# Kernel tuning notes

Hardware: AMD Instinct MI355X
Metric: run time of the kernel (lower is better)

The kernel has to match this reference:

```python
import jax, jax.numpy as jnp
import numpy as np

N_NODES = 10000
N_EDGES = 100000
MUL = 32        # multiplicity of 0e and 1o in node feats / out irreps
ATTR = 16       # node_attrs scalars
RADIAL = 8      # edge_feats scalars
W_NUMEL = 4 * MUL * MUL  # 4 CG paths, fully-connected [mul1=32, mul2=1, mul_out=32]


def setup_inputs() -> dict:
    key = jax.random.key(0)
    ks = jax.random.split(key, 12)
    return {
        'node_attrs': jax.random.normal(ks[0], (N_NODES, ATTR), jnp.float32),
        'node_feats': jax.random.normal(ks[1], (N_NODES, 4 * MUL), jnp.float32),  # 32x0e | 32x1o flattened
        'edge_attrs': jax.random.normal(ks[2], (N_EDGES, 4), jnp.float32),        # Y0 | Y1 (3 comps)
        'edge_feats': jax.random.normal(ks[3], (N_EDGES, RADIAL), jnp.float32),
        'edge_index': jax.random.randint(ks[4], (2, N_EDGES), 0, N_NODES, jnp.int32),
        'Wgen': jax.random.normal(ks[5], (RADIAL, W_NUMEL), jnp.float32),  # conv_tp_weights (o3.Linear on scalars)
        'L1s': jax.random.normal(ks[6], (MUL, MUL), jnp.float32),  # linear_1, scalar block
        'L1v': jax.random.normal(ks[7], (MUL, MUL), jnp.float32),  # linear_1, vector block
        'WS0': jax.random.normal(ks[8], (MUL, ATTR, MUL), jnp.float32),  # skip_tp 0e*0e->0e
        'WS1': jax.random.normal(ks[9], (MUL, ATTR, MUL), jnp.float32),  # skip_tp 1o*0e->1o
        'L2s': jax.random.normal(ks[10], (MUL, MUL), jnp.float32),
        'L2v': jax.random.normal(ks[11], (MUL, MUL), jnp.float32),
    }


def reference(node_attrs, node_feats, edge_attrs, edge_feats, edge_index,
              Wgen, L1s, L1v, WS0, WS1, L2s, L2v):
    sender, receiver = edge_index[0], edge_index[1]
    n = node_attrs.shape[0]

    # gather sender node feats, split irreps: [E,32] scalars, [E,32,3] vectors
    g = node_feats[sender]
    xs = g[:, :MUL]
    xv = g[:, MUL:].reshape(-1, MUL, 3)
    ys = edge_attrs[:, 0]    # l=0 edge attr
    yv = edge_attrs[:, 1:]   # l=1 edge attr, [E,3]

    # per-edge generated tensor-product weights (o3.Linear on scalar edge feats)
    tw = (edge_feats @ Wgen) * (1.0 / np.sqrt(RADIAL))
    tw = tw.reshape(-1, 4, MUL, MUL)
    WA, WB, WC, WD = tw[:, 0], tw[:, 1], tw[:, 2], tw[:, 3]

    # fully-connected CG tensor product (4 paths, edge attrs have mul=1)
    outA = jnp.einsum('euw,eu,e->ew', WA, xs, ys)          # 0e x 0e -> 0e
    outB = jnp.einsum('euw,eu,ei->ewi', WB, xs, yv)        # 0e x 1o -> 1o
    outC = jnp.einsum('euw,eui,e->ewi', WC, xv, ys)        # 1o x 0e -> 1o
    dot = jnp.einsum('eui,ei->eu', xv, yv) * (1.0 / np.sqrt(3.0))  # CG for 1o x 1o -> 0e
    outD = jnp.einsum('euw,eu->ew', WD, dot)
    alpha = 1.0 / np.sqrt(2 * MUL)  # fan-in path normalization (2 paths x mul1=32 per output irrep)
    ms = (outA + outD) * alpha      # [E,32]
    mv = (outB + outC) * alpha      # [E,32,3]

    # linear_1 (per-irrep mixing)
    lnorm = 1.0 / np.sqrt(MUL)
    ms = (ms @ L1s) * lnorm
    mv = jnp.einsum('ewi,wu->eui', mv, L1v) * lnorm

    # scatter-sum messages to receiver nodes
    Ms = jax.ops.segment_sum(ms, receiver, num_segments=n)   # [N,32]
    Mv = jax.ops.segment_sum(mv, receiver, num_segments=n)   # [N,32,3]

    # skip_tp: out irreps x node_attrs (16x0e) -> out irreps
    snorm = 1.0 / np.sqrt(MUL * ATTR)
    ss = jnp.einsum('uvw,nu,nv->nw', WS0, Ms, node_attrs) * snorm
    sv = jnp.einsum('uvw,nui,nv->nwi', WS1, Mv, node_attrs) * snorm

    # linear_2
    ss = (ss @ L2s) * lnorm
    sv = jnp.einsum('nwi,wu->nui', sv, L2v) * lnorm

    # residual, flatten irreps back to [N, 128]
    return jnp.concatenate([Ms + ss, (Mv + sv).reshape(n, 3 * MUL)], axis=1)
```

## Files before the change

### kernel.cpp

```cpp
#include <hip/hip_runtime.h>
#include <hip/hip_bf16.h>

#define N_NODES 10000
#define N_EDGES 100000
#define SLOTS 40

typedef __attribute__((ext_vector_type(8))) short short8;
typedef __attribute__((ext_vector_type(4))) short shortx4;
typedef __attribute__((ext_vector_type(4))) float f32x4;

static __device__ inline short bf16bits(float x) {
    union { __bf16 b; short s; } u;
    u.b = (__bf16)x;
    return u.s;
}
static __device__ inline unsigned short bf16u(float x) {
    union { __bf16 b; unsigned short s; } u;
    u.b = (__bf16)x;
    return u.s;
}
static __device__ inline float bf2f(unsigned short us) {
    union { unsigned int u; float f; } c;
    c.u = ((unsigned int)us) << 16;
    return c.f;
}
static __device__ inline short8 cvt8(const float* f) {
    short8 r;
#pragma unroll
    for (int j = 0; j < 8; ++j) r[j] = bf16bits(f[j]);
    return r;
}

__global__ __launch_bounds__(1024) void prep_kernel(
    const float* __restrict__ Wgen, const float* __restrict__ L1s,
    const float* __restrict__ L1v, const float* __restrict__ WS0,
    const float* __restrict__ WS1, const float* __restrict__ L2s,
    const float* __restrict__ L2v, unsigned short* __restrict__ Wc,
    unsigned short* __restrict__ WB0, unsigned short* __restrict__ WB1,
    int* __restrict__ cnt) {
    const float S = 1.0f / 128.0f;
    int tid = blockIdx.x * 1024 + threadIdx.x;
    if (tid < N_NODES) cnt[tid] = 0;
    if (tid < 32768) {
        int j = tid & 7;
        int lane = (tid >> 3) & 63;
        int ks = (tid >> 9) & 7;
        int nt = tid >> 12;
        int col = nt * 16 + (lane & 15);
        int u = (lane >> 4) * 8 + j;
        int r = ks;
        int p, c2;
        const float* M;
        float sc = S;
        if (col < 32)      { p = 0; M = L1s; c2 = col; }
        else if (col < 64) { p = 1; M = L1v; c2 = col - 32; }
        else if (col < 96) { p = 2; M = L1v; c2 = col - 64; }
        else               { p = 3; M = L1s; c2 = col - 96; sc = S * 0.57735026918962576f; }
        const float* wg = Wgen + r * 4096 + p * 1024 + u * 32;
        float acc = 0.f;
#pragma unroll
        for (int w = 0; w < 32; ++w) acc += wg[w] * M[w * 32 + c2];
        Wc[tid] = bf16u(acc * sc);
    } else {
        int idx = tid - 32768;
        int table = idx >> 14;
        int r14 = idx & 16383;
        int j = r14 & 7;
        int lane = (r14 >> 3) & 63;
        int ks = (r14 >> 9) & 15;
        int k = ks * 32 + (lane >> 4) * 8 + j;
        int u = k >> 4, v = k & 15;
        int w = ((r14 >> 13) & 1) * 16 + (lane & 15);
        const float* WS = table ? WS1 : WS0;
        const float* L2 = table ? L2v : L2s;
        const float* src = WS + u * 512 + v * 32;
        float acc = 0.f;
#pragma unroll
        for (int x = 0; x < 32; ++x) acc += src[x] * L2[x * 32 + w];
        unsigned short val = bf16u(acc * S);
        if (table) WB1[r14] = val; else WB0[r14] = val;
    }
}

__global__ __launch_bounds__(256) void edge_kernel(
    const float* __restrict__ node_feats, const float* __restrict__ edge_attrs,
    const float* __restrict__ edge_feats, const int* __restrict__ edge_index,
    const unsigned short* __restrict__ Wc, int* __restrict__ cnt,
    unsigned short* __restrict__ Msg) {
    __shared__ short8 sW8[4096];
    __shared__ int sSL[4][16];
    __shared__ f32x4 sEA[4][16];
    {
        const short8* src = (const short8*)Wc;
        for (int i = threadIdx.x; i < 4096; i += 256) sW8[i] = src[i];
    }
    __syncthreads();

    const int lane = threadIdx.x & 63;
    const int m = lane & 15, q = lane >> 4;
    const int wv = threadIdx.x >> 6;
    const int wave = (blockIdx.x * 256 + threadIdx.x) >> 6;
    const int stride = gridDim.x * 4;
    const int NT = N_EDGES / 16;

    int tile = wave;
    if (tile >= NT) return;

    float xsC[8], xvC[24], efC[8];
    f32x4 eaC;
    int slC = 0;

    {
        int e = tile * 16 + m;
        int snd = edge_index[e];
        if (lane < 16) {
            int r = edge_index[N_EDGES + e];
            slC = r * SLOTS + atomicAdd(&cnt[r], 1);
        }
        const float* g = node_feats + snd * 128;
        *(f32x4*)&xsC[0] = *(const f32x4*)(g + q * 8);
        *(f32x4*)&xsC[4] = *(const f32x4*)(g + q * 8 + 4);
#pragma unroll
        for (int i = 0; i < 6; ++i)
            *(f32x4*)&xvC[i * 4] = *(const f32x4*)(g + 32 + q * 24 + i * 4);
        *(f32x4*)&efC[0] = *(const f32x4*)(edge_feats + e * 8);
        *(f32x4*)&efC[4] = *(const f32x4*)(edge_feats + e * 8 + 4);
        eaC = *(const f32x4*)(edge_attrs + e * 4);
    }
    int snd1 = 0, rcv1 = 0;
    {
        int t1 = tile + stride;
        if (t1 < NT) {
            int e1 = t1 * 16 + m;
            snd1 = edge_index[e1];
            if (lane < 16) rcv1 = edge_index[N_EDGES + e1];
        }
    }

    while (tile < NT) {
        const int tn = tile + stride;
        const bool hasN = tn < NT;
        const int t2 = tile + 2 * stride;
        const bool has2 = t2 < NT;

        if (lane < 16) {
            sSL[wv][lane] = slC;
            sEA[wv][lane] = eaC;
        }

        float xsN[8], xvN[24], efN[8];
        f32x4 eaN;
        int slN = 0;
        if (hasN) {
            int en = tn * 16 + m;
            if (lane < 16) slN = rcv1 * SLOTS + atomicAdd(&cnt[rcv1], 1);
            const float* gN = node_feats + snd1 * 128;
            *(f32x4*)&xsN[0] = *(const f32x4*)(gN + q * 8);
            *(f32x4*)&xsN[4] = *(const f32x4*)(gN + q * 8 + 4);
#pragma unroll
            for (int i = 0; i < 6; ++i)
                *(f32x4*)&xvN[i * 4] = *(const f32x4*)(gN + 32 + q * 24 + i * 4);
            *(f32x4*)&efN[0] = *(const f32x4*)(edge_feats + en * 8);
            *(f32x4*)&efN[4] = *(const f32x4*)(edge_feats + en * 8 + 4);
            eaN = *(const f32x4*)(edge_attrs + en * 4);
        }

        int snd2 = 0, rcv2 = 0;
        if (has2) {
            int e2 = t2 * 16 + m;
            snd2 = edge_index[e2];
            if (lane < 16) rcv2 = edge_index[N_EDGES + e2];
        }

        float dt[8];
        {
            float y0 = eaC.y, y1 = eaC.z, y2 = eaC.w;
#pragma unroll
            for (int j = 0; j < 8; ++j)
                dt[j] = xvC[j * 3] * y0 + xvC[j * 3 + 1] * y1 + xvC[j * 3 + 2] * y2;
        }

        f32x4 z = {0.f, 0.f, 0.f, 0.f};
        f32x4 fA[2] = {z, z}, fB[2] = {z, z}, fD[2] = {z, z};
        f32x4 fC[3][2] = {{z, z}, {z, z}, {z, z}};

#pragma unroll
        for (int ks = 0; ks < 8; ++ks) {
            float h = efC[ks];
            float t[8];
#pragma unroll
            for (int j = 0; j < 8; ++j) t[j] = h * xsC[j];
            {
                short8 a = cvt8(t);
                fA[0] = __builtin_amdgcn_mfma_f32_16x16x32_bf16(a, sW8[(0 * 8 + ks) * 64 + lane], fA[0], 0, 0, 0);
                fA[1] = __builtin_amdgcn_mfma_f32_16x16x32_bf16(a, sW8[(1 * 8 + ks) * 64 + lane], fA[1], 0, 0, 0);
                fB[0] = __builtin_amdgcn_mfma_f32_16x16x32_bf16(a, sW8[(2 * 8 + ks) * 64 + lane], fB[0], 0, 0, 0);
                fB[1] = __builtin_amdgcn_mfma_f32_16x16x32_bf16(a, sW8[(3 * 8 + ks) * 64 + lane], fB[1], 0, 0, 0);
            }
            {
                short8 bc0 = sW8[(4 * 8 + ks) * 64 + lane];
                short8 bc1 = sW8[(5 * 8 + ks) * 64 + lane];
#pragma unroll
                for (int c = 0; c < 3; ++c) {
#pragma unroll
                    for (int j = 0; j < 8; ++j) t[j] = h * xvC[j * 3 + c];
                    short8 a = cvt8(t);
                    fC[c][0] = __builtin_amdgcn_mfma_f32_16x16x32_bf16(a, bc0, fC[c][0], 0, 0, 0);
                    fC[c][1] = __builtin_amdgcn_mfma_f32_16x16x32_bf16(a, bc1, fC[c][1], 0, 0, 0);
                }
            }
            {
#pragma unroll
                for (int j = 0; j < 8; ++j) t[j] = h * dt[j];
                short8 a = cvt8(t);
                fD[0] = __builtin_amdgcn_mfma_f32_16x16x32_bf16(a, sW8[(6 * 8 + ks) * 64 + lane], fD[0], 0, 0, 0);
                fD[1] = __builtin_amdgcn_mfma_f32_16x16x32_bf16(a, sW8[(7 * 8 + ks) * 64 + lane], fD[1], 0, 0, 0);
            }
        }

        int4 sl4 = *(const int4*)&sSL[wv][q * 4];
        const int slR[4] = {sl4.x, sl4.y, sl4.z, sl4.w};
#pragma unroll
        for (int t4 = 0; t4 < 4; ++t4) {
            f32x4 ea4 = sEA[wv][q * 4 + t4];
            float ysr = ea4.x, y0r = ea4.y, y1r = ea4.z, y2r = ea4.w;
            int dr = slR[t4];
#pragma unroll
            for (int nt = 0; nt < 2; ++nt) {
                int col = nt * 16 + m;
                float pb = fB[nt][t4];
                shortx4 pk;
                pk[0] = bf16bits(ysr * fA[nt][t4] + fD[nt][t4]);
                pk[1] = bf16bits(y0r * pb + ysr * fC[0][nt][t4]);
                pk[2] = bf16bits(y1r * pb + ysr * fC[1][nt][t4]);
                pk[3] = bf16bits(y2r * pb + ysr * fC[2][nt][t4]);
                *(shortx4*)(Msg + (size_t)dr * 128 + col * 4) = pk;
            }
        }

        tile = tn;
        if (hasN) {
#pragma unroll
            for (int j = 0; j < 8; ++j) { xsC[j] = xsN[j]; efC[j] = efN[j]; }
#pragma unroll
            for (int j = 0; j < 24; ++j) xvC[j] = xvN[j];
            eaC = eaN;
            slC = slN;
            snd1 = snd2;
            rcv1 = rcv2;
        }
    }
}

__global__ __launch_bounds__(256) void node_kernel(
    const float* __restrict__ node_attrs, const unsigned short* __restrict__ Msg,
    const int* __restrict__ cnt, const unsigned short* __restrict__ WB0,
    const unsigned short* __restrict__ WB1, float* __restrict__ out) {
    __shared__ float sM[16][129];
    __shared__ float sAt[16][17];
    int n0 = blockIdx.x * 16;

    int nl = threadIdx.x >> 4;
    int cg = threadIdx.x & 15;
    int n = n0 + nl;
    int s0 = n * SLOTS;
    int s1 = s0 + cnt[n];
    float acc[8];
#pragma unroll
    for (int j = 0; j < 8; ++j) acc[j] = 0.f;
    int s = s0;
    for (; s + 3 < s1; s += 4) {
        f32x4 r0 = *(const f32x4*)(Msg + (size_t)(s + 0) * 128 + cg * 8);
        f32x4 r1 = *(const f32x4*)(Msg + (size_t)(s + 1) * 128 + cg * 8);
        f32x4 r2 = *(const f32x4*)(Msg + (size_t)(s + 2) * 128 + cg * 8);
        f32x4 r3 = *(const f32x4*)(Msg + (size_t)(s + 3) * 128 + cg * 8);
        const unsigned short* u0 = (const unsigned short*)&r0;
        const unsigned short* u1 = (const unsigned short*)&r1;
        const unsigned short* u2 = (const unsigned short*)&r2;
        const unsigned short* u3 = (const unsigned short*)&r3;
#pragma unroll
        for (int j = 0; j < 8; ++j)
            acc[j] += (bf2f(u0[j]) + bf2f(u1[j])) + (bf2f(u2[j]) + bf2f(u3[j]));
    }
    for (; s < s1; ++s) {
        f32x4 raw = *(const f32x4*)(Msg + (size_t)s * 128 + cg * 8);
        const unsigned short* us = (const unsigned short*)&raw;
#pragma unroll
        for (int j = 0; j < 8; ++j) acc[j] += bf2f(us[j]);
    }
#pragma unroll
    for (int j = 0; j < 8; ++j)
        sM[nl][(j & 3) * 32 + cg * 2 + (j >> 2)] = acc[j];
    sAt[nl][cg] = node_attrs[n * 16 + cg];
    __syncthreads();

    int p = threadIdx.x >> 6;
    int lane = threadIdx.x & 63;
    int m = lane & 15, q = lane >> 4;
    const unsigned short* WB = (p == 0) ? WB0 : WB1;
    int chb = p * 32;
    f32x4 z = {0.f, 0.f, 0.f, 0.f};
    f32x4 D0 = z, D1 = z;
#pragma unroll
    for (int ks = 0; ks < 16; ++ks) {
        int kb = ks * 32 + q * 8;
        float t[8];
#pragma unroll
        for (int j = 0; j < 8; ++j) {
            int k = kb + j;
            t[j] = sM[m][chb + (k >> 4)] * sAt[m][k & 15];
        }
        short8 a = cvt8(t);
        short8 b0 = *(const short8*)(WB + (ks * 64 + lane) * 8);
        short8 b1 = *(const short8*)(WB + ((16 + ks) * 64 + lane) * 8);
        D0 = __builtin_amdgcn_mfma_f32_16x16x32_bf16(a, b0, D0, 0, 0, 0);
        D1 = __builtin_amdgcn_mfma_f32_16x16x32_bf16(a, b1, D1, 0, 0, 0);
    }

#pragma unroll
    for (int t4 = 0; t4 < 4; ++t4) {
        int nl2 = q * 4 + t4;
        int nn = n0 + nl2;
        if (p == 0) {
            out[nn * 128 + m]      = sM[nl2][m] + D0[t4];
            out[nn * 128 + 16 + m] = sM[nl2][16 + m] + D1[t4];
        } else {
            int i = p - 1;
            out[nn * 128 + 32 + m * 3 + i]        = sM[nl2][chb + m] + D0[t4];
            out[nn * 128 + 32 + (16 + m) * 3 + i] = sM[nl2][chb + 16 + m] + D1[t4];
        }
    }
}

extern "C" void kernel_launch(void* const* d_in, const int* in_sizes, int n_in,
                              void* d_out, int out_size, void* d_ws, size_t ws_size,
                              hipStream_t stream) {
    (void)in_sizes; (void)n_in; (void)out_size; (void)ws_size;
    const float* node_attrs = (const float*)d_in[0];
    const float* node_feats = (const float*)d_in[1];
    const float* edge_attrs = (const float*)d_in[2];
    const float* edge_feats = (const float*)d_in[3];
    const int*   edge_index = (const int*)d_in[4];
    const float* Wgen = (const float*)d_in[5];
    const float* L1s  = (const float*)d_in[6];
    const float* L1v  = (const float*)d_in[7];
    const float* WS0  = (const float*)d_in[8];
    const float* WS1  = (const float*)d_in[9];
    const float* L2s  = (const float*)d_in[10];
    const float* L2v  = (const float*)d_in[11];
    float* out = (float*)d_out;
    char* ws = (char*)d_ws;

    unsigned short* Msg = (unsigned short*)ws;
    unsigned short* Wc  = (unsigned short*)(ws + 102400000);
    unsigned short* WB0 = (unsigned short*)(ws + 102465536);
    unsigned short* WB1 = (unsigned short*)(ws + 102498304);
    int* cnt = (int*)(ws + 102531072);

    prep_kernel<<<64, 1024, 0, stream>>>(Wgen, L1s, L1v, WS0, WS1, L2s, L2v,
                                         Wc, WB0, WB1, cnt);
    edge_kernel<<<512, 256, 0, stream>>>(node_feats, edge_attrs, edge_feats,
                                         edge_index, Wc, cnt, Msg);
    node_kernel<<<625, 256, 0, stream>>>(node_attrs, Msg, cnt, WB0, WB1, out);
}
```

Measured before the change: 131.1 us.

## Switch MFMA operands and messages from bf16 to fp16 with packed scaling

Replaces bf16 with fp16 across the prep, edge and node kernels. Sender features are converted to packed fp16 once per tile, and each radial step is applied with packed half multiplies instead of eight float multiplies plus per-element bf16 conversions. The node reduction also gets an 8-way unrolled gather loop. The aim is to cut VALU conversion work in the edge inner loop, at the cost of fp16 range limits (overflow risk on large products) and rounding of the radial factor to half precision.

```diff
diff --git a/kernel.cpp b/kernel.cpp
--- a/kernel.cpp
+++ b/kernel.cpp
@@ -1,34 +1,45 @@
 #include <hip/hip_runtime.h>
-#include <hip/hip_bf16.h>
 
 #define N_NODES 10000
 #define N_EDGES 100000
 #define SLOTS 40
 
-typedef __attribute__((ext_vector_type(8))) short short8;
-typedef __attribute__((ext_vector_type(4))) short shortx4;
+typedef __attribute__((ext_vector_type(8))) _Float16 f16x8;
+typedef __attribute__((ext_vector_type(2))) _Float16 f16x2;
 typedef __attribute__((ext_vector_type(4))) float f32x4;
 
-static __device__ inline short bf16bits(float x) {
-    union { __bf16 b; short s; } u;
-    u.b = (__bf16)x;
+static __device__ inline f16x2 pkrtz(float a, float b) {
+    auto t = __builtin_amdgcn_cvt_pkrtz(a, b);
+    union { decltype(t) x; f16x2 y; } u;
+    u.x = t;
+    return u.y;
+}
+static __device__ inline unsigned short f16u(float x) {
+    union { _Float16 h; unsigned short s; } u;
+    u.h = (_Float16)x;
     return u.s;
 }
-static __device__ inline unsigned short bf16u(float x) {
-    union { __bf16 b; unsigned short s; } u;
-    u.b = (__bf16)x;
-    return u.s;
-}
-static __device__ inline float bf2f(unsigned short us) {
-    union { unsigned int u; float f; } c;
-    c.u = ((unsigned int)us) << 16;
-    return c.f;
-}
-static __device__ inline short8 cvt8(const float* f) {
-    short8 r;
-#pragma unroll
-    for (int j = 0; j < 8; ++j) r[j] = bf16bits(f[j]);
+static __device__ inline float f16f(unsigned short us) {
+    union { unsigned short s; _Float16 h; } u;
+    u.s = us;
+    return (float)u.h;
+}
+static __device__ inline f16x8 cvt8h(const float* f) {
+    f16x8 r; f16x2* rp = (f16x2*)&r;
+#pragma unroll
+    for (int i = 0; i < 4; ++i) rp[i] = pkrtz(f[2 * i], f[2 * i + 1]);
     return r;
+}
+static __device__ inline f16x8 scale8(f16x2 h2, f16x8 x) {
+    f16x8 r; f16x2* rp = (f16x2*)&r; f16x2* xp = (f16x2*)&x;
+#pragma unroll
+    for (int i = 0; i < 4; ++i) rp[i] = h2 * xp[i];
+    return r;
+}
+static __device__ inline int pack2(float a, float b) {
+    union { f16x2 h; int i; } u;
+    u.h = pkrtz(a, b);
+    return u.i;
 }
 
 __global__ __launch_bounds__(1024) void prep_kernel(
@@ -60,7 +71,7 @@
         float acc = 0.f;
 #pragma unroll
         for (int w = 0; w < 32; ++w) acc += wg[w] * M[w * 32 + c2];
-        Wc[tid] = bf16u(acc * sc);
+        Wc[tid] = f16u(acc * sc);
     } else {
         int idx = tid - 32768;
         int table = idx >> 14;
@@ -77,7 +88,7 @@
         float acc = 0.f;
 #pragma unroll
         for (int x = 0; x < 32; ++x) acc += src[x] * L2[x * 32 + w];
-        unsigned short val = bf16u(acc * S);
+        unsigned short val = f16u(acc * S);
         if (table) WB1[r14] = val; else WB0[r14] = val;
     }
 }
@@ -87,11 +98,11 @@
     const float* __restrict__ edge_feats, const int* __restrict__ edge_index,
     const unsigned short* __restrict__ Wc, int* __restrict__ cnt,
     unsigned short* __restrict__ Msg) {
-    __shared__ short8 sW8[4096];
+    __shared__ f16x8 sW8[4096];
     __shared__ int sSL[4][16];
     __shared__ f32x4 sEA[4][16];
     {
-        const short8* src = (const short8*)Wc;
+        const f16x8* src = (const f16x8*)Wc;
         for (int i = threadIdx.x; i < 4096; i += 256) sW8[i] = src[i];
     }
     __syncthreads();
@@ -106,7 +117,8 @@
     int tile = wave;
     if (tile >= NT) return;
 
-    float xsC[8], xvC[24], efC[8];
+    f16x8 xs8, xv8[3], dt8;
+    float efC[8];
     f32x4 eaC;
     int slC = 0;
 
@@ -118,14 +130,30 @@
             slC = r * SLOTS + atomicAdd(&cnt[r], 1);
         }
         const float* g = node_feats + snd * 128;
-        *(f32x4*)&xsC[0] = *(const f32x4*)(g + q * 8);
-        *(f32x4*)&xsC[4] = *(const f32x4*)(g + q * 8 + 4);
+        float xs[8], xv[24];
+        *(f32x4*)&xs[0] = *(const f32x4*)(g + q * 8);
+        *(f32x4*)&xs[4] = *(const f32x4*)(g + q * 8 + 4);
 #pragma unroll
         for (int i = 0; i < 6; ++i)
-            *(f32x4*)&xvC[i * 4] = *(const f32x4*)(g + 32 + q * 24 + i * 4);
+            *(f32x4*)&xv[i * 4] = *(const f32x4*)(g + 32 + q * 24 + i * 4);
         *(f32x4*)&efC[0] = *(const f32x4*)(edge_feats + e * 8);
         *(f32x4*)&efC[4] = *(const f32x4*)(edge_feats + e * 8 + 4);
         eaC = *(const f32x4*)(edge_attrs + e * 4);
+        float dt[8];
+        float y0 = eaC.y, y1 = eaC.z, y2 = eaC.w;
+#pragma unroll
+        for (int j = 0; j < 8; ++j)
+            dt[j] = xv[j * 3] * y0 + xv[j * 3 + 1] * y1 + xv[j * 3 + 2] * y2;
+        xs8 = cvt8h(xs);
+#pragma unroll
+        for (int c = 0; c < 3; ++c) {
+            f16x8 r; f16x2* rp = (f16x2*)&r;
+#pragma unroll
+            for (int i = 0; i < 4; ++i)
+                rp[i] = pkrtz(xv[(2 * i) * 3 + c], xv[(2 * i + 1) * 3 + c]);
+            xv8[c] = r;
+        }
+        dt8 = cvt8h(dt);
     }
     int snd1 = 0, rcv1 = 0;
     {
@@ -172,49 +200,35 @@
             if (lane < 16) rcv2 = edge_index[N_EDGES + e2];
         }
 
-        float dt[8];
-        {
-            float y0 = eaC.y, y1 = eaC.z, y2 = eaC.w;
-#pragma unroll
-            for (int j = 0; j < 8; ++j)
-                dt[j] = xvC[j * 3] * y0 + xvC[j * 3 + 1] * y1 + xvC[j * 3 + 2] * y2;
-        }
-
         f32x4 z = {0.f, 0.f, 0.f, 0.f};
         f32x4 fA[2] = {z, z}, fB[2] = {z, z}, fD[2] = {z, z};
         f32x4 fC[3][2] = {{z, z}, {z, z}, {z, z}};
 
 #pragma unroll
         for (int ks = 0; ks < 8; ++ks) {
-            float h = efC[ks];
-            float t[8];
-#pragma unroll
-            for (int j = 0; j < 8; ++j) t[j] = h * xsC[j];
+            _Float16 h = (_Float16)efC[ks];
+            f16x2 h2 = {h, h};
             {
-                short8 a = cvt8(t);
-                fA[0] = __builtin_amdgcn_mfma_f32_16x16x32_bf16(a, sW8[(0 * 8 + ks) * 64 + lane], fA[0], 0, 0, 0);
-                fA[1] = __builtin_amdgcn_mfma_f32_16x16x32_bf16(a, sW8[(1 * 8 + ks) * 64 + lane], fA[1], 0, 0, 0);
-                fB[0] = __builtin_amdgcn_mfma_f32_16x16x32_bf16(a, sW8[(2 * 8 + ks) * 64 + lane], fB[0], 0, 0, 0);
-                fB[1] = __builtin_amdgcn_mfma_f32_16x16x32_bf16(a, sW8[(3 * 8 + ks) * 64 + lane], fB[1], 0, 0, 0);
+                f16x8 a = scale8(h2, xs8);
+                fA[0] = __builtin_amdgcn_mfma_f32_16x16x32_f16(a, sW8[(0 * 8 + ks) * 64 + lane], fA[0], 0, 0, 0);
+                fA[1] = __builtin_amdgcn_mfma_f32_16x16x32_f16(a, sW8[(1 * 8 + ks) * 64 + lane], fA[1], 0, 0, 0);
+                fB[0] = __builtin_amdgcn_mfma_f32_16x16x32_f16(a, sW8[(2 * 8 + ks) * 64 + lane], fB[0], 0, 0, 0);
+                fB[1] = __builtin_amdgcn_mfma_f32_16x16x32_f16(a, sW8[(3 * 8 + ks) * 64 + lane], fB[1], 0, 0, 0);
             }
             {
-                short8 bc0 = sW8[(4 * 8 + ks) * 64 + lane];
-                short8 bc1 = sW8[(5 * 8 + ks) * 64 + lane];
+                f16x8 bc0 = sW8[(4 * 8 + ks) * 64 + lane];
+                f16x8 bc1 = sW8[(5 * 8 + ks) * 64 + lane];
 #pragma unroll
                 for (int c = 0; c < 3; ++c) {
-#pragma unroll
-                    for (int j = 0; j < 8; ++j) t[j] = h * xvC[j * 3 + c];
-                    short8 a = cvt8(t);
-                    fC[c][0] = __builtin_amdgcn_mfma_f32_16x16x32_bf16(a, bc0, fC[c][0], 0, 0, 0);
-                    fC[c][1] = __builtin_amdgcn_mfma_f32_16x16x32_bf16(a, bc1, fC[c][1], 0, 0, 0);
+                    f16x8 a = scale8(h2, xv8[c]);
+                    fC[c][0] = __builtin_amdgcn_mfma_f32_16x16x32_f16(a, bc0, fC[c][0], 0, 0, 0);
+                    fC[c][1] = __builtin_amdgcn_mfma_f32_16x16x32_f16(a, bc1, fC[c][1], 0, 0, 0);
                 }
             }
             {
-#pragma unroll
-                for (int j = 0; j < 8; ++j) t[j] = h * dt[j];
-                short8 a = cvt8(t);
-                fD[0] = __builtin_amdgcn_mfma_f32_16x16x32_bf16(a, sW8[(6 * 8 + ks) * 64 + lane], fD[0], 0, 0, 0);
-                fD[1] = __builtin_amdgcn_mfma_f32_16x16x32_bf16(a, sW8[(7 * 8 + ks) * 64 + lane], fD[1], 0, 0, 0);
+                f16x8 a = scale8(h2, dt8);
+                fD[0] = __builtin_amdgcn_mfma_f32_16x16x32_f16(a, sW8[(6 * 8 + ks) * 64 + lane], fD[0], 0, 0, 0);
+                fD[1] = __builtin_amdgcn_mfma_f32_16x16x32_f16(a, sW8[(7 * 8 + ks) * 64 + lane], fD[1], 0, 0, 0);
             }
         }
 
@@ -229,21 +243,34 @@
             for (int nt = 0; nt < 2; ++nt) {
                 int col = nt * 16 + m;
                 float pb = fB[nt][t4];
-                shortx4 pk;
-                pk[0] = bf16bits(ysr * fA[nt][t4] + fD[nt][t4]);
-                pk[1] = bf16bits(y0r * pb + ysr * fC[0][nt][t4]);
-                pk[2] = bf16bits(y1r * pb + ysr * fC[1][nt][t4]);
-                pk[3] = bf16bits(y2r * pb + ysr * fC[2][nt][t4]);
-                *(shortx4*)(Msg + (size_t)dr * 128 + col * 4) = pk;
+                int2 pk;
+                pk.x = pack2(ysr * fA[nt][t4] + fD[nt][t4],
+                             y0r * pb + ysr * fC[0][nt][t4]);
+                pk.y = pack2(y1r * pb + ysr * fC[1][nt][t4],
+                             y2r * pb + ysr * fC[2][nt][t4]);
+                *(int2*)(Msg + (size_t)dr * 128 + col * 4) = pk;
             }
         }
 
         tile = tn;
         if (hasN) {
-#pragma unroll
-            for (int j = 0; j < 8; ++j) { xsC[j] = xsN[j]; efC[j] = efN[j]; }
-#pragma unroll
-            for (int j = 0; j < 24; ++j) xvC[j] = xvN[j];
+            float dtN[8];
+            float y0 = eaN.y, y1 = eaN.z, y2 = eaN.w;
+#pragma unroll
+            for (int j = 0; j < 8; ++j)
+                dtN[j] = xvN[j * 3] * y0 + xvN[j * 3 + 1] * y1 + xvN[j * 3 + 2] * y2;
+            xs8 = cvt8h(xsN);
+#pragma unroll
+            for (int c = 0; c < 3; ++c) {
+                f16x8 r; f16x2* rp = (f16x2*)&r;
+#pragma unroll
+                for (int i = 0; i < 4; ++i)
+                    rp[i] = pkrtz(xvN[(2 * i) * 3 + c], xvN[(2 * i + 1) * 3 + c]);
+                xv8[c] = r;
+            }
+            dt8 = cvt8h(dtN);
+#pragma unroll
+            for (int j = 0; j < 8; ++j) efC[j] = efN[j];
             eaC = eaN;
             slC = slN;
             snd1 = snd2;
@@ -269,6 +296,20 @@
 #pragma unroll
     for (int j = 0; j < 8; ++j) acc[j] = 0.f;
     int s = s0;
+    for (; s + 7 < s1; s += 8) {
+        f32x4 r[8];
+#pragma unroll
+        for (int i = 0; i < 8; ++i)
+            r[i] = *(const f32x4*)(Msg + (size_t)(s + i) * 128 + cg * 8);
+#pragma unroll
+        for (int j = 0; j < 8; ++j) {
+            float a = 0.f;
+#pragma unroll
+            for (int i = 0; i < 8; ++i)
+                a += f16f(((const unsigned short*)&r[i])[j]);
+            acc[j] += a;
+        }
+    }
     for (; s + 3 < s1; s += 4) {
         f32x4 r0 = *(const f32x4*)(Msg + (size_t)(s + 0) * 128 + cg * 8);
         f32x4 r1 = *(const f32x4*)(Msg + (size_t)(s + 1) * 128 + cg * 8);
@@ -280,13 +321,13 @@
         const unsigned short* u3 = (const unsigned short*)&r3;
 #pragma unroll
         for (int j = 0; j < 8; ++j)
-            acc[j] += (bf2f(u0[j]) + bf2f(u1[j])) + (bf2f(u2[j]) + bf2f(u3[j]));
+            acc[j] += (f16f(u0[j]) + f16f(u1[j])) + (f16f(u2[j]) + f16f(u3[j]));
     }
     for (; s < s1; ++s) {
         f32x4 raw = *(const f32x4*)(Msg + (size_t)s * 128 + cg * 8);
         const unsigned short* us = (const unsigned short*)&raw;
 #pragma unroll
-        for (int j = 0; j < 8; ++j) acc[j] += bf2f(us[j]);
+        for (int j = 0; j < 8; ++j) acc[j] += f16f(us[j]);
     }
 #pragma unroll
     for (int j = 0; j < 8; ++j)
@@ -310,11 +351,11 @@
             int k = kb + j;
             t[j] = sM[m][chb + (k >> 4)] * sAt[m][k & 15];
         }
-        short8 a = cvt8(t);
-        short8 b0 = *(const short8*)(WB + (ks * 64 + lane) * 8);
-        short8 b1 = *(const short8*)(WB + ((16 + ks) * 64 + lane) * 8);
-        D0 = __builtin_amdgcn_mfma_f32_16x16x32_bf16(a, b0, D0, 0, 0, 0);
-        D1 = __builtin_amdgcn_mfma_f32_16x16x32_bf16(a, b1, D1, 0, 0, 0);
+        f16x8 a = cvt8h(t);
+        f16x8 b0 = *(const f16x8*)(WB + (ks * 64 + lane) * 8);
+        f16x8 b1 = *(const f16x8*)(WB + ((16 + ks) * 64 + lane) * 8);
+        D0 = __builtin_amdgcn_mfma_f32_16x16x32_f16(a, b0, D0, 0, 0, 0);
+        D1 = __builtin_amdgcn_mfma_f32_16x16x32_f16(a, b1, D1, 0, 0, 0);
     }
 
 #pragma unroll
```

New measurement: 127.3 us, median of 2. -2.9%, faster.
